# Performance work log

Hardware: AMD Instinct MI355X
Metric: run time of the kernel (lower is better)

## Reference

```python
import jax, jax.numpy as jnp
import numpy as np

N = 10000            # nodes
E = 320000           # edges (avg degree 32)
L = 4                # layers
S = 64               # hidden 0e multiplicity
V = 16               # hidden 1o multiplicity
EMB = 32             # node-attr embedding dim
NB = 8               # bessel basis per channel (r and v -> 2*NB edge feats)
MR = 2.5             # max_radius
DEG = 32.0           # num_neighbors
GS = S + V           # gate input scalars: 64 scalars + 16 gates
NW = S * 2 + V * 2 + V * 2   # 192 per-edge tensor-product weights
MAXT = 100           # max atom types


def _semi_unitary(K):
    # Newton-Schulz orthogonalization: K^T K -> I (semi-unitary uplift matrix)
    K = K / jnp.linalg.norm(K)
    for _ in range(10):
        K = 1.5 * K - 0.5 * K @ (K.T @ K)
    return K


def _smooth_cutoff(t):
    u = 2.0 * (t - 1.0)
    y = (1.0 - jnp.cos(jnp.pi * u)) * 0.5
    return jnp.where(u > 0, 0.0, jnp.where(u < -1.0, 1.0, y))


def _edge_geom(d):
    # d: (E,3) edge vector. Returns cutoff-weighted 1x1o SH (component norm) and bessel features.
    r = jnp.linalg.norm(d, axis=1)                       # (E,)
    sh = np.sqrt(3.0) * d / r[:, None]                   # spherical harmonics 1x1o
    attr = _smooth_cutoff(r / MR)[:, None] * sh          # (E,3)
    k = jnp.arange(1, NB + 1, dtype=jnp.float32) * jnp.pi
    feat = np.sqrt(2.0 / MR) * jnp.sin(k * (r / MR)[:, None]) / r[:, None]
    return attr, feat * np.sqrt(NB)                      # (E,3), (E,NB)


def _fctp(s, v, attr, Ws, Wv):
    # FullyConnectedTensorProduct with pure-scalar (0e) node attr == attr-weighted per-irrep linear
    os = jnp.einsum('ni,ne,oie->no', s, attr, Ws) / np.sqrt(s.shape[1] * EMB)
    ov = jnp.einsum('nim,ne,oie->nom', v, attr, Wv) / np.sqrt(v.shape[1] * EMB)
    return os, ov


def _forward(x, node_attr, edge_src, edge_dst, emb_table, PU_K, h, mix,
             si_Ws, si_Wv, sc_Ws, sc_Wv, lin1_Ws, lin1_Wv, lin2_Ws, lin2_Wv,
             fc_W1, fc_b1, fc_W2, fc_b2, fc_W3, fc_b3):
    attr = emb_table[node_attr]                          # (N,EMB)
    K = _semi_unitary(PU_K)                              # (V,2)
    yv = jnp.einsum('ui,nim->num', K, x.reshape(N, 2, 3))  # uplift vectors
    ys = jnp.zeros((N, S), x.dtype)
    ys_old, yv_old = ys, yv
    c_s, c_x = np.sin(np.pi / 8), np.cos(np.pi / 8)
    for i in range(L):
        ar, fr = _edge_geom(x[:, :3][edge_src] - x[:, :3][edge_dst])
        av, fv = _edge_geom(x[:, 3:][edge_src] - x[:, 3:][edge_dst])
        a = jnp.stack([ar, av], axis=1)                  # (E,2,3) = 2x1o edge attr
        ef = jnp.concatenate([fr, fv], axis=1)           # (E,2*NB)
        # radial MLP -> per-edge TP weights
        hd = jax.nn.silu(ef @ fc_W1[i] + fc_b1[i])
        hd = jax.nn.silu(hd @ fc_W2[i] + fc_b2[i])
        w = hd @ fc_W3[i] + fc_b3[i]                     # (E,NW)
        w1 = w[:, :S * 2].reshape(-1, S, 2)
        w2 = w[:, S * 2:S * 2 + V * 2].reshape(-1, V, 2)
        w3 = w[:, S * 2 + V * 2:].reshape(-1, V, 2)
        # conv: lin1 -> gather -> TP -> scatter -> lin2 ; plus self-connection
        fs, fvv = _fctp(ys, yv, attr, lin1_Ws[i], lin1_Wv[i])
        s_src, v_src = fs[edge_src], fvv[edge_src]
        # 0e x 1o -> 1o (uvu)
        o1 = jnp.einsum('euv,eu,evm->eum', w1, s_src, a) / np.sqrt(2.0)   # (E,S,3)
        # 1o x 1o -> 0e (uvu)
        dots = jnp.einsum('eum,evm->euv', v_src, a)
        o2 = jnp.einsum('euv,euv->eu', w2, dots) / np.sqrt(6.0)           # (E,V)
        # 1o x 1o -> 1o (cross, uvu)
        cr = jnp.cross(v_src[:, :, None, :], a[:, None, :, :])            # (E,V,2,3)
        o3 = jnp.einsum('euv,euvm->eum', w3, cr) / 2.0                    # (E,V,3)
        mid_s = jax.ops.segment_sum(o2, edge_dst, num_segments=N) / np.sqrt(DEG)
        mid_v = jax.ops.segment_sum(jnp.concatenate([o1, o3], axis=1), edge_dst,
                                    num_segments=N) / np.sqrt(DEG)        # (N,S+V,3)
        cs2, cv2 = _fctp(mid_s, mid_v, attr, lin2_Ws[i], lin2_Wv[i])      # (N,GS),(N,V,3)
        scs, scv = _fctp(ys, yv, attr, sc_Ws[i], sc_Wv[i])
        conv_s = c_s * scs + c_x * cs2
        conv_v = c_s * scv + c_x * cv2
        # gate: silu scalars, sigmoid gates * gated vectors
        gns = jax.nn.silu(conv_s[:, :S])
        gnv = jax.nn.sigmoid(conv_s[:, S:])[:, :, None] * conv_v
        # self-interaction: per-irrep linear
        sis = ys @ si_Ws[i].T / np.sqrt(S)
        siv = jnp.einsum('oi,nim->nom', si_Wv[i], yv) / np.sqrt(V)
        # leapfrog update
        h2 = h[i] ** 2
        ns = 2.0 * ys - ys_old + h2 * (mix[i] * gns + (mix[i] - 1.0) * sis)
        nv = 2.0 * yv - yv_old + h2 * (mix[i] * gnv + (mix[i] - 1.0) * siv)
        ys_old, yv_old = ys, yv
        ys, yv = ns, nv
        x = jnp.einsum('ui,num->nim', K, yv).reshape(N, 6)   # project
    return x


def setup_inputs() -> dict:
    key = jax.random.key(0)
    ks = jax.random.split(key, 24)
    def g(i, sh, fan=1.0):
        return jax.random.normal(ks[i], sh, dtype=jnp.float32) / np.sqrt(fan)
    edge_src = jax.random.randint(ks[20], (E,), 0, N, dtype=jnp.int32)
    off = jax.random.randint(ks[21], (E,), 1, N, dtype=jnp.int32)
    edge_dst = (edge_src + off) % N                      # guarantees src != dst
    return {
        'x': g(0, (N, 6)),
        'batch': jnp.zeros((N,), jnp.int32),
        'node_attr': jax.random.randint(ks[22], (N,), 0, MAXT, dtype=jnp.int32),
        'edge_src': edge_src,
        'edge_dst': edge_dst,
        'emb_table': g(1, (MAXT, EMB)),
        'PU_K': g(2, (V, 2)),
        'h': jnp.full((L,), 0.01, jnp.float32),
        'mix': jnp.full((L,), 0.5, jnp.float32),
        'si_Ws': g(3, (L, S, S)), 'si_Wv': g(4, (L, V, V)),
        'sc_Ws': g(5, (L, GS, S, EMB)), 'sc_Wv': g(6, (L, V, V, EMB)),
        'lin1_Ws': g(7, (L, S, S, EMB)), 'lin1_Wv': g(8, (L, V, V, EMB)),
        'lin2_Ws': g(9, (L, GS, V, EMB)), 'lin2_Wv': g(10, (L, V, S + V, EMB)),
        'fc_W1': g(11, (L, 2 * NB, 64), 2 * NB), 'fc_b1': jnp.zeros((L, 64), jnp.float32),
        'fc_W2': g(12, (L, 64, 64), 64), 'fc_b2': jnp.zeros((L, 64), jnp.float32),
        'fc_W3': g(13, (L, 64, NW), 64), 'fc_b3': jnp.zeros((L, NW), jnp.float32),
    }


def reference(x, batch, node_attr, edge_src, edge_dst, emb_table, PU_K, h, mix,
              si_Ws, si_Wv, sc_Ws, sc_Wv, lin1_Ws, lin1_Wv, lin2_Ws, lin2_Wv,
              fc_W1, fc_b1, fc_W2, fc_b2, fc_W3, fc_b3):
    return _forward(x, node_attr, edge_src, edge_dst, emb_table, PU_K, h, mix,
                    si_Ws, si_Wv, sc_Ws, sc_Wv, lin1_Ws, lin1_Wv, lin2_Ws, lin2_Wv,
                    fc_W1, fc_b1, fc_W2, fc_b2, fc_W3, fc_b3)
```

## Files before the change

### kernel.cpp

```cpp
#include <hip/hip_runtime.h>
#include <hip/hip_fp8.h>
#include <math.h>

#define NN 10000
#define NE 320000
#define PI_F 3.14159265358979323846f

typedef __attribute__((ext_vector_type(8))) short short8x;
typedef __attribute__((ext_vector_type(4))) float float4x;
typedef __attribute__((ext_vector_type(4))) unsigned short ushort4x;

#if defined(__has_builtin)
#if __has_builtin(__builtin_amdgcn_cvt_pk_fp8_f32) && __has_builtin(__builtin_amdgcn_cvt_f32_fp8)
#define HW_FP8 1
#endif
#endif

__device__ __forceinline__ unsigned short f2b(float f) {
    unsigned b = __float_as_uint(f);
    return (unsigned short)((b + 0x7FFFu + ((b >> 16) & 1u)) >> 16);
}
__device__ __forceinline__ float b2f(unsigned short u) {
    return __uint_as_float(((unsigned)u) << 16);
}
__device__ __forceinline__ float silu(float x) {
    return x / (1.f + __expf(-x));
}
__device__ __forceinline__ unsigned char f2e4(float f) {
#ifdef HW_FP8
    int r = __builtin_amdgcn_cvt_pk_fp8_f32(f, f, 0, false);
    return (unsigned char)(r & 0xff);
#else
    __hip_fp8_e4m3 q(f);
    return (unsigned char)q.__x;
#endif
}
__device__ __forceinline__ float e42f(unsigned char v) {
#ifdef HW_FP8
    return __builtin_amdgcn_cvt_f32_fp8((int)v, 0);
#else
    __hip_fp8_e4m3 q;
    q.__x = (__hip_fp8_storage_t)v;
    return (float)q;
#endif
}
__device__ __forceinline__ float e4sel(unsigned word, int sel) {
#ifdef HW_FP8
    switch (sel & 3) {
        case 0:  return __builtin_amdgcn_cvt_f32_fp8((int)word, 0);
        case 1:  return __builtin_amdgcn_cvt_f32_fp8((int)word, 1);
        case 2:  return __builtin_amdgcn_cvt_f32_fp8((int)word, 2);
        default: return __builtin_amdgcn_cvt_f32_fp8((int)word, 3);
    }
#else
    return e42f((unsigned char)((word >> (8*(sel & 3))) & 0xffu));
#endif
}
__device__ __forceinline__ unsigned pk4(float a, float b, float c, float d) {
#ifdef HW_FP8
    unsigned w = (unsigned)__builtin_amdgcn_cvt_pk_fp8_f32(a, b, 0, false);
    w = (unsigned)__builtin_amdgcn_cvt_pk_fp8_f32(c, d, (int)w, true);
    return w;
#else
    return (unsigned)f2e4(a) | ((unsigned)f2e4(b) << 8) |
           ((unsigned)f2e4(c) << 16) | ((unsigned)f2e4(d) << 24);
#endif
}

__global__ void k_newton_kernel(const float* __restrict__ PU, float* __restrict__ Kout)
{
    if (threadIdx.x != 0 || blockIdx.x != 0) return;
    float K[32];
    float nrm = 0.f;
    for (int i = 0; i < 32; ++i) { K[i] = PU[i]; nrm += K[i]*K[i]; }
    float inv = 1.0f / sqrtf(nrm);
    for (int i = 0; i < 32; ++i) K[i] *= inv;
    for (int it = 0; it < 10; ++it) {
        float m00 = 0.f, m01 = 0.f, m11 = 0.f;
        for (int u = 0; u < 16; ++u) {
            float a = K[2*u], b = K[2*u+1];
            m00 += a*a; m01 += a*b; m11 += b*b;
        }
        for (int u = 0; u < 16; ++u) {
            float a = K[2*u], b = K[2*u+1];
            K[2*u]   = 1.5f*a - 0.5f*(a*m00 + b*m01);
            K[2*u+1] = 1.5f*b - 0.5f*(a*m01 + b*m11);
        }
    }
    for (int i = 0; i < 32; ++i) Kout[i] = K[i];
}

__global__ __launch_bounds__(256) void init_all_kernel(
    const float* __restrict__ x, const float* __restrict__ K,
    float* __restrict__ xp, float* __restrict__ yv0, float* __restrict__ yv1,
    float* __restrict__ ys0, float* __restrict__ ys1, float* __restrict__ fsb)
{
    int tid = blockIdx.x*256 + threadIdx.x;
    if (tid < NN*8) {
        int n = tid >> 3, c = tid & 7;
        xp[tid] = (c < 6) ? x[n*6 + c] : 0.f;
        return;
    }
    int t2 = tid - NN*8;
    if (t2 < NN*48) {
        int n = t2/48, j = t2%48, u = j/3, m = j%3;
        float v = K[2*u]*x[n*6+m] + K[2*u+1]*x[n*6+3+m];
        yv0[t2] = v; yv1[t2] = v;
        return;
    }
    t2 -= NN*48;
    if (t2 < NN*64) { ys0[t2] = 0.f; ys1[t2] = 0.f; fsb[t2] = 0.f; }
}

__global__ void init_fvv_kernel(const float* __restrict__ yv, const int* __restrict__ types,
                                const float* __restrict__ lin1vT0, float* __restrict__ fvv)
{
    int tid = blockIdx.x*blockDim.x + threadIdx.x;
    if (tid >= NN*48) return;
    int n = tid/48, j = tid%48, o = j/3, m = j%3;
    int t = types[n];
    const float* W = lin1vT0 + (size_t)t*256;
    float acc = 0.f;
    #pragma unroll
    for (int i = 0; i < 16; ++i) acc += yv[n*48 + i*3 + m]*W[i*16 + o];
    fvv[tid] = acc;
}

__device__ __forceinline__ void be_body(const float* __restrict__ W, const float* __restrict__ emb,
                                        float* __restrict__ out, int id, int O, int I, float scale)
{
    int o = id % O; int r = id / O;
    int i = r % I; r /= I;
    int t = r % 100; int l = r / 100;
    const float* w  = W + (((size_t)l*O + o)*I + i)*32;
    const float* em = emb + (size_t)t*32;
    float acc = 0.f;
    #pragma unroll
    for (int e = 0; e < 32; ++e) acc += w[e]*em[e];
    out[id] = acc*scale;
}

#define PREP_TOTAL (2048000 + 1638400 + 512000 + 512000 + 102400 + 102400 + 49152 + 16384 + 16384 + 8192 + 1024)
__global__ __launch_bounds__(256) void prep_kernel(
    const float* __restrict__ lin1_Ws, const float* __restrict__ lin1_Wv,
    const float* __restrict__ sc_Ws,   const float* __restrict__ sc_Wv,
    const float* __restrict__ lin2_Ws, const float* __restrict__ lin2_Wv,
    const float* __restrict__ si_Ws,   const float* __restrict__ si_Wv,
    const float* __restrict__ fc_W1,   const float* __restrict__ fc_W2,
    const float* __restrict__ fc_W3,   const float* __restrict__ emb,
    float* __restrict__ lin1sT, float* __restrict__ lin1vT,
    float* __restrict__ scsT,   float* __restrict__ scvT,
    float* __restrict__ lin2sT, float* __restrict__ lin2vT,
    float* __restrict__ siWsT,  float* __restrict__ siWvT,
    unsigned short* __restrict__ w1bp, unsigned short* __restrict__ w2bp,
    unsigned short* __restrict__ w3bf)
{
    const float s2048 = 0.022097086912079608f;
    const float s512  = 0.044194173824159216f;
    const float s2560 = 0.019764235376052372f;
    int tid = blockIdx.x*256 + threadIdx.x;
    if (tid < 2048000) { be_body(sc_Ws,   emb, scsT,   tid, 80, 64, s2048); return; }
    tid -= 2048000;
    if (tid < 1638400) { be_body(lin1_Ws, emb, lin1sT, tid, 64, 64, s2048); return; }
    tid -= 1638400;
    if (tid < 512000)  { be_body(lin2_Ws, emb, lin2sT, tid, 80, 16, s512);  return; }
    tid -= 512000;
    if (tid < 512000)  { be_body(lin2_Wv, emb, lin2vT, tid, 16, 80, s2560); return; }
    tid -= 512000;
    if (tid < 102400)  { be_body(lin1_Wv, emb, lin1vT, tid, 16, 16, s512);  return; }
    tid -= 102400;
    if (tid < 102400)  { be_body(sc_Wv,   emb, scvT,   tid, 16, 16, s512);  return; }
    tid -= 102400;
    if (tid < 49152) {
        int o = tid % 64; int r = tid / 64; int i = r % 192; int l = r / 192;
        w3bf[tid] = f2b(fc_W3[((size_t)l*64 + o)*192 + i]);
        return;
    }
    tid -= 49152;
    if (tid < 16384) {
        int o = tid % 64; int r = tid / 64; int i = r % 64; int l = r / 64;
        siWsT[tid] = si_Ws[((size_t)l*64 + o)*64 + i]*0.125f;
        return;
    }
    tid -= 16384;
    if (tid < 16384) {
        int kk = tid % 64; int r = tid / 64; int n = r % 64; int l = r / 64;
        w2bp[tid] = f2b(fc_W2[((size_t)l*64 + kk)*64 + n]);
        return;
    }
    tid -= 16384;
    if (tid < 8192) {
        int kk = tid % 32; int r = tid / 32; int n = r % 64; int l = r / 64;
        float v = (kk < 16) ? fc_W1[((size_t)l*16 + kk)*64 + n] : 0.f;
        w1bp[tid] = f2b(v);
        return;
    }
    tid -= 8192;
    if (tid < 1024) {
        int o = tid % 16; int r = tid / 16; int i = r % 16; int l = r / 16;
        siWvT[tid] = si_Wv[((size_t)l*16 + o)*16 + i]*0.25f;
    }
}

__global__ void hist_kernel(const int* __restrict__ dst, int* __restrict__ deg)
{
    int e = blockIdx.x*256 + threadIdx.x;
    if (e < NE) atomicAdd(&deg[dst[e]], 1);
}

__global__ __launch_bounds__(256) void scan_kernel(const int* __restrict__ deg,
                                                   int* __restrict__ segoff,
                                                   int* __restrict__ cursor)
{
    __shared__ int part[256];
    int tid = threadIdx.x;
    int base = tid*40;
    int s = 0;
    for (int i = 0; i < 40; ++i) { int idx = base+i; if (idx < NN) s += deg[idx]; }
    part[tid] = s;
    __syncthreads();
    for (int o = 1; o < 256; o <<= 1) {
        int v = (tid >= o) ? part[tid-o] : 0;
        __syncthreads();
        part[tid] += v;
        __syncthreads();
    }
    int excl = part[tid] - s;
    for (int i = 0; i < 40; ++i) {
        int idx = base+i;
        if (idx < NN) { segoff[idx] = excl; cursor[idx] = excl; excl += deg[idx]; }
        else if (idx == NN) { segoff[NN] = excl; }
    }
}

__global__ void scatter_kernel(const int* __restrict__ src, const int* __restrict__ dst,
                               int* __restrict__ cursor,
                               int* __restrict__ srcs, int* __restrict__ dsts)
{
    int e = blockIdx.x*256 + threadIdx.x;
    if (e >= NE) return;
    int d = dst[e];
    int p = atomicAdd(&cursor[d], 1);
    srcs[p] = src[e]; dsts[p] = d;
}

__global__ __launch_bounds__(256, 5) void edge_fused_kernel(
    const float* __restrict__ xp,
    const int* __restrict__ srcs, const int* __restrict__ dsts,
    const unsigned short* __restrict__ w1b,
    const float* __restrict__ b1,
    const unsigned short* __restrict__ w2b,
    const float* __restrict__ b2,
    const unsigned short* __restrict__ w3b,
    const float* __restrict__ b3,
    const float* __restrict__ fs, const float* __restrict__ fvv,
    float* __restrict__ mid)
{
    __shared__ __align__(16) unsigned char smem[192*68];
    __shared__ unsigned short fsl[64][68];
    __shared__ unsigned short fvl[48][68];
    __shared__ float abuf[6][68];
    __shared__ int sdst[64];
    __shared__ unsigned smaskl[2];
    unsigned short* hbuf = (unsigned short*)smem;
    const float C3f = 0.08838834764831845f;
    int lane = threadIdx.x & 63;
    int wid  = threadIdx.x >> 6;
    int eblk = blockIdx.x * 64;
    int row16 = lane & 15, quad = lane >> 4;
    int erow = 16*wid + row16;

    if (threadIdx.x < 64) {
        int tid = threadIdx.x;
        int own = dsts[eblk + tid];
        int pidx = eblk + tid - ((tid > 0) ? 1 : 0);
        int prev = dsts[pidx];
        sdst[tid] = own;
        bool nb = (tid > 0) && (own != prev);
        unsigned long long bm = __ballot(nb);
        if (tid == 0) { smaskl[0] = (unsigned)bm; smaskl[1] = (unsigned)(bm >> 32); }
    }

    if (lane < 32) {
        int eidx = 16*wid + (lane & 15);
        int half = lane >> 4;
        int p = eblk + eidx;
        int s = srcs[p], d = dsts[p];
        int off = 3*half;
        const float* xs = xp + (size_t)s*8 + off;
        const float* xd = xp + (size_t)d*8 + off;
        float d0 = xs[0]-xd[0], d1 = xs[1]-xd[1], d2 = xs[2]-xd[2];
        float r = sqrtf(d0*d0 + d1*d1 + d2*d2);
        float invr = 1.0f/r;
        float u = 0.8f*r - 2.0f;
        float cut = (u > 0.f) ? 0.f : ((u < -1.f) ? 1.f : 0.5f*(1.f - __cosf(PI_F*u)));
        float sc = 1.7320508075688772f*cut*invr;
        abuf[off+0][eidx] = sc*d0;
        abuf[off+1][eidx] = sc*d1;
        abuf[off+2][eidx] = sc*d2;
        float fsc = 2.5298221281347035f*invr;
        float wr = 1.2566370614359172f*r;
        unsigned epk[4];
        #pragma unroll
        for (int k = 0; k < 4; ++k) {
            float e0 = fsc*__sinf((float)(2*k+1)*wr);
            float e1 = fsc*__sinf((float)(2*k+2)*wr);
            epk[k] = (unsigned)f2b(e0) | ((unsigned)f2b(e1) << 16);
        }
        uint4* hr = (uint4*)(hbuf + eidx*72);
        uint4 q; q.x = epk[0]; q.y = epk[1]; q.z = epk[2]; q.w = epk[3];
        hr[half] = q;
        uint4 qz; qz.x = 0; qz.y = 0; qz.z = 0; qz.w = 0;
        hr[2+half] = qz;
    } else {
        int eidx = 16*wid + (lane & 15);
        int half = (lane >> 4) & 1;
        int s = srcs[eblk + eidx];
        const float4* fp = (const float4*)(fs + (size_t)s*64 + half*32);
        #pragma unroll
        for (int g = 0; g < 8; ++g) {
            float4 t = fp[g];
            int u0 = half*32 + g*4;
            fsl[u0+0][eidx] = f2b(t.x*0.125f);
            fsl[u0+1][eidx] = f2b(t.y*0.125f);
            fsl[u0+2][eidx] = f2b(t.z*0.125f);
            fsl[u0+3][eidx] = f2b(t.w*0.125f);
        }
        const float4* vp = (const float4*)(fvv + (size_t)s*48 + half*24);
        #pragma unroll
        for (int g = 0; g < 6; ++g) {
            float4 t = vp[g];
            int j0 = half*24 + g*4;
            fvl[j0+0][eidx] = f2b(t.x*C3f);
            fvl[j0+1][eidx] = f2b(t.y*C3f);
            fvl[j0+2][eidx] = f2b(t.z*C3f);
            fvl[j0+3][eidx] = f2b(t.w*C3f);
        }
    }

    {
        short8x a = *(const short8x*)(hbuf + erow*72 + quad*8);
        float4x c[4];
        #pragma unroll
        for (int nt = 0; nt < 4; ++nt) {
            short8x b = *(const short8x*)(w1b + ((size_t)(nt*16 + row16))*32 + quad*8);
            c[nt] = __builtin_amdgcn_mfma_f32_16x16x32_bf16(a, b, (float4x){0.f,0.f,0.f,0.f}, 0, 0, 0);
        }
        #pragma unroll
        for (int nt = 0; nt < 4; ++nt) {
            float bias = b1[nt*16 + row16];
            #pragma unroll
            for (int r = 0; r < 4; ++r) {
                float h = silu(c[nt][r] + bias);
                hbuf[(16*wid + quad*4 + r)*72 + nt*16 + row16] = f2b(h);
            }
        }
    }
    {
        short8x a0v = *(const short8x*)(hbuf + erow*72 + 0*32 + quad*8);
        short8x a1v = *(const short8x*)(hbuf + erow*72 + 1*32 + quad*8);
        float4x c[4];
        #pragma unroll
        for (int nt = 0; nt < 4; ++nt) {
            short8x b0 = *(const short8x*)(w2b + ((size_t)(nt*16 + row16))*64 + 0*32 + quad*8);
            float4x t = __builtin_amdgcn_mfma_f32_16x16x32_bf16(a0v, b0, (float4x){0.f,0.f,0.f,0.f}, 0, 0, 0);
            short8x b1v = *(const short8x*)(w2b + ((size_t)(nt*16 + row16))*64 + 1*32 + quad*8);
            c[nt] = __builtin_amdgcn_mfma_f32_16x16x32_bf16(a1v, b1v, t, 0, 0, 0);
        }
        #pragma unroll
        for (int nt = 0; nt < 4; ++nt) {
            float bias = b2[nt*16 + row16];
            #pragma unroll
            for (int r = 0; r < 4; ++r) {
                float h = silu(c[nt][r] + bias);
                hbuf[(16*wid + quad*4 + r)*72 + nt*16 + row16] = f2b(h);
            }
        }
    }
    {
        short8x a0v = *(const short8x*)(hbuf + erow*72 + 0*32 + quad*8);
        short8x a1v = *(const short8x*)(hbuf + erow*72 + 1*32 + quad*8);
        __syncthreads();
        float4x acc[12];
        #pragma unroll
        for (int nt = 0; nt < 12; ++nt) {
            short8x b0 = *(const short8x*)(w3b + ((size_t)(nt*16 + row16))*64 + 0*32 + quad*8);
            float4x t = __builtin_amdgcn_mfma_f32_16x16x32_bf16(a0v, b0, (float4x){0.f,0.f,0.f,0.f}, 0, 0, 0);
            short8x b1v = *(const short8x*)(w3b + ((size_t)(nt*16 + row16))*64 + 1*32 + quad*8);
            acc[nt] = __builtin_amdgcn_mfma_f32_16x16x32_bf16(a1v, b1v, t, 0, 0, 0);
        }
        #pragma unroll
        for (int nt = 0; nt < 12; ++nt) {
            unsigned pw = pk4(acc[nt][0], acc[nt][1], acc[nt][2], acc[nt][3]);
            *(unsigned*)(smem + (size_t)(nt*16 + row16)*68 + 16*wid + quad*4) = pw;
        }
    }
    __syncthreads();

    {
        int c = threadIdx.x;
        unsigned mk0 = __builtin_amdgcn_readfirstlane(smaskl[0]);
        unsigned mk1 = __builtin_amdgcn_readfirstlane(smaskl[1]);
        float acc = 0.f;
        int dcur = sdst[0];
        if (c < 192) {
            int u = c / 3;
            int m = c - 3*u;
            const unsigned char* wra = smem + (size_t)(2*u)*68;
            const unsigned char* wrb = wra + 68;
            const unsigned short* fsr = &fsl[u][0];
            const float* a0r = &abuf[m][0];
            const float* a1r = &abuf[3+m][0];
            float bA = b3[2*u], bB = b3[2*u+1];
            for (int e4 = 0; e4 < 64; e4 += 4) {
                unsigned wa4 = *(const unsigned*)(wra + e4);
                unsigned wb4 = *(const unsigned*)(wrb + e4);
                ushort4x f4v = *(const ushort4x*)(fsr + e4);
                float4x a04 = *(const float4x*)(a0r + e4);
                float4x a14 = *(const float4x*)(a1r + e4);
                float q0 = b2f(f4v[0])*((e4sel(wa4,0)+bA)*a04[0] + (e4sel(wb4,0)+bB)*a14[0]);
                float q1 = b2f(f4v[1])*((e4sel(wa4,1)+bA)*a04[1] + (e4sel(wb4,1)+bB)*a14[1]);
                float q2 = b2f(f4v[2])*((e4sel(wa4,2)+bA)*a04[2] + (e4sel(wb4,2)+bB)*a14[2]);
                float q3 = b2f(f4v[3])*((e4sel(wa4,3)+bA)*a04[3] + (e4sel(wb4,3)+bB)*a14[3]);
                unsigned mch = ((e4 < 32) ? (mk0 >> e4) : (mk1 >> (e4-32))) & 15u;
                if (mch == 0) {
                    acc += (q0 + q1) + (q2 + q3);
                } else {
                    float q[4] = {q0, q1, q2, q3};
                    #pragma unroll
                    for (int k = 0; k < 4; ++k) {
                        if (mch & (1u<<k)) {
                            atomicAdd(&mid[(size_t)dcur*256 + c], acc);
                            acc = 0.f; dcur = sdst[e4+k];
                        }
                        acc += q[k];
                    }
                }
            }
            atomicAdd(&mid[(size_t)dcur*256 + c], acc);
        } else if (c < 208) {
            int u = c - 192;
            const unsigned char* wra = smem + (size_t)(128 + 2*u)*68;
            const unsigned char* wrb = wra + 68;
            const unsigned short* v0r = &fvl[3*u+0][0];
            const unsigned short* v1r = &fvl[3*u+1][0];
            const unsigned short* v2r = &fvl[3*u+2][0];
            float bA = b3[128 + 2*u], bB = b3[129 + 2*u];
            const float FS = 0.8164965809277259f;
            for (int e4 = 0; e4 < 64; e4 += 4) {
                unsigned wa4 = *(const unsigned*)(wra + e4);
                unsigned wb4 = *(const unsigned*)(wrb + e4);
                ushort4x v04 = *(const ushort4x*)(v0r + e4);
                ushort4x v14 = *(const ushort4x*)(v1r + e4);
                ushort4x v24 = *(const ushort4x*)(v2r + e4);
                float4x a00 = *(const float4x*)(&abuf[0][e4]);
                float4x a01 = *(const float4x*)(&abuf[1][e4]);
                float4x a02 = *(const float4x*)(&abuf[2][e4]);
                float4x a10 = *(const float4x*)(&abuf[3][e4]);
                float4x a11 = *(const float4x*)(&abuf[4][e4]);
                float4x a12 = *(const float4x*)(&abuf[5][e4]);
                float q[4];
                #pragma unroll
                for (int k = 0; k < 4; ++k) {
                    float v0 = b2f(v04[k]), v1 = b2f(v14[k]), v2 = b2f(v24[k]);
                    float dd0 = v0*a00[k] + v1*a01[k] + v2*a02[k];
                    float dd1 = v0*a10[k] + v1*a11[k] + v2*a12[k];
                    q[k] = (e4sel(wa4,k)+bA)*dd0 + (e4sel(wb4,k)+bB)*dd1;
                }
                unsigned mch = ((e4 < 32) ? (mk0 >> e4) : (mk1 >> (e4-32))) & 15u;
                if (mch == 0) {
                    acc += (q[0] + q[1]) + (q[2] + q[3]);
                } else {
                    #pragma unroll
                    for (int k = 0; k < 4; ++k) {
                        if (mch & (1u<<k)) {
                            atomicAdd(&mid[(size_t)dcur*256 + c], acc*FS);
                            acc = 0.f; dcur = sdst[e4+k];
                        }
                        acc += q[k];
                    }
                }
            }
            atomicAdd(&mid[(size_t)dcur*256 + c], acc*FS);
        } else {
            int j = c - 208;
            int u = j / 3;
            int m = j - 3*u;
            int m1 = (m == 2) ? 0 : (m + 1);
            int m2 = 3 - m - m1;
            const unsigned char* wra = smem + (size_t)(160 + 2*u)*68;
            const unsigned char* wrb = wra + 68;
            const unsigned short* var = &fvl[3*u+m1][0];
            const unsigned short* vbr = &fvl[3*u+m2][0];
            const float* am1a = &abuf[m1][0];
            const float* am2a = &abuf[m2][0];
            const float* am1b = &abuf[3+m1][0];
            const float* am2b = &abuf[3+m2][0];
            float bA = b3[160 + 2*u], bB = b3[161 + 2*u];
            for (int e4 = 0; e4 < 64; e4 += 4) {
                unsigned wa4 = *(const unsigned*)(wra + e4);
                unsigned wb4 = *(const unsigned*)(wrb + e4);
                ushort4x va4 = *(const ushort4x*)(var + e4);
                ushort4x vb4 = *(const ushort4x*)(vbr + e4);
                float4x a1m1 = *(const float4x*)(am1a + e4);
                float4x a1m2 = *(const float4x*)(am2a + e4);
                float4x a2m1 = *(const float4x*)(am1b + e4);
                float4x a2m2 = *(const float4x*)(am2b + e4);
                float q[4];
                #pragma unroll
                for (int k = 0; k < 4; ++k) {
                    float va = b2f(va4[k]), vb = b2f(vb4[k]);
                    float cx0 = va*a1m2[k] - vb*a1m1[k];
                    float cx1 = va*a2m2[k] - vb*a2m1[k];
                    q[k] = (e4sel(wa4,k)+bA)*cx0 + (e4sel(wb4,k)+bB)*cx1;
                }
                unsigned mch = ((e4 < 32) ? (mk0 >> e4) : (mk1 >> (e4-32))) & 15u;
                if (mch == 0) {
                    acc += (q[0] + q[1]) + (q[2] + q[3]);
                } else {
                    #pragma unroll
                    for (int k = 0; k < 4; ++k) {
                        if (mch & (1u<<k)) {
                            atomicAdd(&mid[(size_t)dcur*256 + c], acc);
                            acc = 0.f; dcur = sdst[e4+k];
                        }
                        acc += q[k];
                    }
                }
            }
            atomicAdd(&mid[(size_t)dcur*256 + c], acc);
        }
    }
}

__global__ __launch_bounds__(256) void node_update_kernel(
    const float* __restrict__ ys, const float* __restrict__ yv,
    float* __restrict__ ys_old, float* __restrict__ yv_old,
    const float* __restrict__ mid,
    const int* __restrict__ types,
    const float* __restrict__ scsT, const float* __restrict__ scvT,
    const float* __restrict__ lin2sT, const float* __restrict__ lin2vT,
    const float* __restrict__ siWsT, const float* __restrict__ siWvT,
    const float* __restrict__ lin1sTn, const float* __restrict__ lin1vTn,
    const float* __restrict__ Kbuf,
    const float* __restrict__ hv, const float* __restrict__ mixv, int layer,
    float* __restrict__ fs_out, float* __restrict__ fvv_out,
    float* __restrict__ xpad, float* __restrict__ dout)
{
    int n = blockIdx.x;
    int lane = threadIdx.x;
    __shared__ float ys_l[64], yv_l[48], mids[16], midv[240];
    __shared__ float conv_s[80], conv_v[48], sis_l[64], siv_l[48], ysn[64], yvn[48];
    int t = types[n];
    {
        float v = mid[(size_t)n*256 + lane];
        if (lane < 192) midv[lane] = v;
        else if (lane < 208) mids[lane-192] = v;
        else midv[192 + (lane-208)] = v;
    }
    if (lane < 64) ys_l[lane] = ys[n*64 + lane];
    else if (lane < 112) yv_l[lane-64] = yv[n*48 + (lane-64)];
    __syncthreads();
    if (lane < 80) {
        const float* Wsc = scsT + (size_t)t*5120;
        const float* W2s = lin2sT + (size_t)t*1280;
        float a_sc = 0.f, a_2 = 0.f;
        #pragma unroll
        for (int i = 0; i < 64; ++i) a_sc += ys_l[i]*Wsc[i*80 + lane];
        #pragma unroll
        for (int i = 0; i < 16; ++i) a_2 += mids[i]*W2s[i*80 + lane];
        conv_s[lane] = 0.3826834323650898f*a_sc + 0.9238795325112867f*a_2;
    } else if (lane < 144) {
        int o = lane - 80;
        float a_si = 0.f;
        #pragma unroll
        for (int i = 0; i < 64; ++i) a_si += ys_l[i]*siWsT[i*64 + o];
        sis_l[o] = a_si;
    } else if (lane < 192) {
        int j = lane - 144, o = j/3, m = j%3;
        const float* Wsc = scvT + (size_t)t*256;
        const float* W2v = lin2vT + (size_t)t*1280;
        float a_sc = 0.f, a_2 = 0.f, a_si = 0.f;
        #pragma unroll
        for (int i = 0; i < 16; ++i) {
            float y = yv_l[i*3+m];
            a_sc += y*Wsc[i*16+o];
            a_si += y*siWvT[i*16+o];
        }
        #pragma unroll
        for (int i = 0; i < 80; ++i) a_2 += midv[i*3+m]*W2v[i*16+o];
        conv_v[j] = 0.3826834323650898f*a_sc + 0.9238795325112867f*a_2;
        siv_l[j] = a_si;
    }
    __syncthreads();
    float hh = hv[layer]; float h2c = hh*hh; float mx = mixv[layer];
    if (lane < 64) {
        float cs = conv_s[lane];
        float gns = cs/(1.f + __expf(-cs));
        float ns = 2.f*ys_l[lane] - ys_old[n*64+lane] + h2c*(mx*gns + (mx-1.f)*sis_l[lane]);
        ys_old[n*64+lane] = ns;
        ysn[lane] = ns;
    } else if (lane < 112) {
        int j = lane-64, o = j/3;
        float g = 1.f/(1.f + __expf(-conv_s[64+o]));
        float gnv = g*conv_v[j];
        float nv = 2.f*yv_l[j] - yv_old[n*48+j] + h2c*(mx*gnv + (mx-1.f)*siv_l[j]);
        yv_old[n*48+j] = nv;
        yvn[j] = nv;
    }
    __syncthreads();
    if (lane < 6) {
        int i = lane/3, m = lane%3;
        float acc = 0.f;
        #pragma unroll
        for (int u = 0; u < 16; ++u) acc += Kbuf[2*u+i]*yvn[u*3+m];
        xpad[n*8 + lane] = acc;
        if (dout) dout[n*6 + lane] = acc;
    }
    if (lane < 64) {
        const float* W = lin1sTn + (size_t)t*4096;
        float acc = 0.f;
        #pragma unroll
        for (int i = 0; i < 64; ++i) acc += ysn[i]*W[i*64 + lane];
        fs_out[n*64 + lane] = acc;
    } else if (lane < 112) {
        int j = lane - 64, o = j/3, m = j%3;
        const float* W = lin1vTn + (size_t)t*256;
        float acc = 0.f;
        #pragma unroll
        for (int i = 0; i < 16; ++i) acc += yvn[i*3+m]*W[i*16 + o];
        fvv_out[n*48 + j] = acc;
    }
}

extern "C" void kernel_launch(void* const* d_in, const int* in_sizes, int n_in,
                              void* d_out, int out_size, void* d_ws, size_t ws_size,
                              hipStream_t stream)
{
    const float* x_in   = (const float*)d_in[0];
    const int*   types  = (const int*)  d_in[2];
    const int*   esrc   = (const int*)  d_in[3];
    const int*   edst   = (const int*)  d_in[4];
    const float* emb    = (const float*)d_in[5];
    const float* PU     = (const float*)d_in[6];
    const float* hv     = (const float*)d_in[7];
    const float* mixv   = (const float*)d_in[8];
    const float* si_Ws  = (const float*)d_in[9];
    const float* si_Wv  = (const float*)d_in[10];
    const float* sc_Ws  = (const float*)d_in[11];
    const float* sc_Wv  = (const float*)d_in[12];
    const float* lin1_Ws= (const float*)d_in[13];
    const float* lin1_Wv= (const float*)d_in[14];
    const float* lin2_Ws= (const float*)d_in[15];
    const float* lin2_Wv= (const float*)d_in[16];
    const float* fc_W1  = (const float*)d_in[17];
    const float* fc_b1  = (const float*)d_in[18];
    const float* fc_W2  = (const float*)d_in[19];
    const float* fc_b2  = (const float*)d_in[20];
    const float* fc_W3  = (const float*)d_in[21];
    const float* fc_b3  = (const float*)d_in[22];

    float* ws = (float*)d_ws;
    size_t off = 0;
    auto alloc = [&](size_t nf) { float* p = ws + off; off += nf; return p; };
    float* Kbuf   = alloc(64);
    float* x_pad  = alloc(80000);
    float* ys0    = alloc(640000);
    float* ys1    = alloc(640000);
    float* yv0    = alloc(480000);
    float* yv1    = alloc(480000);
    float* fsb    = alloc(640000);
    float* fvvb   = alloc(480000);
    float* midb   = alloc((size_t)NN*256);
    float* lin1sT = alloc((size_t)4*100*4096);
    float* lin1vT = alloc((size_t)4*100*256);
    float* scsT   = alloc((size_t)4*100*5120);
    float* scvT   = alloc((size_t)4*100*256);
    float* lin2sT = alloc((size_t)4*100*1280);
    float* lin2vT = alloc((size_t)4*100*1280);
    float* siWsT  = alloc((size_t)4*4096);
    float* siWvT  = alloc((size_t)4*256);
    int* iws = (int*)(ws + off);
    size_t ioff = 0;
    auto ialloc = [&](size_t ni) { int* p = iws + ioff; ioff += ni; return p; };
    int* deg    = ialloc(NN);
    int* segoff = ialloc(NN + 8);
    int* cursor = ialloc(NN);
    int* srcs   = ialloc(NE);
    int* dsts   = ialloc(NE);
    unsigned short* w1bp = (unsigned short*)(iws + ioff);
    unsigned short* w2bp = w1bp + (size_t)4*64*32;
    unsigned short* w3bf = w2bp + (size_t)4*64*64;

    k_newton_kernel<<<1, 1, 0, stream>>>(PU, Kbuf);
    prep_kernel<<<(PREP_TOTAL + 255)/256, 256, 0, stream>>>(
        lin1_Ws, lin1_Wv, sc_Ws, sc_Wv, lin2_Ws, lin2_Wv, si_Ws, si_Wv,
        fc_W1, fc_W2, fc_W3, emb,
        lin1sT, lin1vT, scsT, scvT, lin2sT, lin2vT, siWsT, siWvT,
        w1bp, w2bp, w3bf);
    {
        int tot = NN*8 + NN*48 + NN*64;
        init_all_kernel<<<(tot + 255)/256, 256, 0, stream>>>(
            x_in, Kbuf, x_pad, yv0, yv1, ys0, ys1, fsb);
    }
    init_fvv_kernel<<<(NN*48 + 255)/256, 256, 0, stream>>>(yv0, types, lin1vT, fvvb);

    (void)hipMemsetAsync(deg, 0, NN*sizeof(int), stream);
    hist_kernel<<<(NE+255)/256, 256, 0, stream>>>(edst, deg);
    scan_kernel<<<1, 256, 0, stream>>>(deg, segoff, cursor);
    scatter_kernel<<<(NE+255)/256, 256, 0, stream>>>(esrc, edst, cursor, srcs, dsts);

    float* ys_cur = ys0; float* ys_old = ys1;
    float* yv_cur = yv0; float* yv_old = yv1;
    for (int l = 0; l < 4; ++l) {
        (void)hipMemsetAsync(midb, 0, (size_t)NN*256*sizeof(float), stream);
        edge_fused_kernel<<<NE/64, 256, 0, stream>>>(
            x_pad, srcs, dsts,
            w1bp + (size_t)l*64*32,  fc_b1 + (size_t)l*64,
            w2bp + (size_t)l*64*64,  fc_b2 + (size_t)l*64,
            w3bf + (size_t)l*192*64, fc_b3 + (size_t)l*192,
            fsb, fvvb, midb);
        int ln = (l + 1) & 3;
        node_update_kernel<<<NN, 256, 0, stream>>>(
            ys_cur, yv_cur, ys_old, yv_old,
            midb, types,
            scsT   + (size_t)l*100*5120, scvT   + (size_t)l*100*256,
            lin2sT + (size_t)l*100*1280, lin2vT + (size_t)l*100*1280,
            siWsT  + (size_t)l*4096,     siWvT  + (size_t)l*256,
            lin1sT + (size_t)ln*100*4096, lin1vT + (size_t)ln*100*256,
            Kbuf, hv, mixv, l, fsb, fvvb,
            x_pad, (l == 3) ? (float*)d_out : nullptr);
        float* tmp;
        tmp = ys_cur; ys_cur = ys_old; ys_old = tmp;
        tmp = yv_cur; yv_cur = yv_old; yv_old = tmp;
    }
}
```

Measured before the change: 936.2 us.

## Split edge-message scatter across waves by edge quarter instead of by output channel

The scatter phase used to give each thread one output channel and loop over all 64 edges, so the three channel groups ran divergent code paths. Now each wave handles a 16-edge quarter, and each lane computes all three m components for one scalar channel plus one vector-path channel. This reuses the bf16 feature and weight loads across the three components and shortens the serial loop per thread. In exchange, segments that cross a quarter boundary produce more atomic adds into mid, and the wave still diverges between the iso2 and cross-product branches.

```diff
diff --git a/kernel.cpp b/kernel.cpp
--- a/kernel.cpp
+++ b/kernel.cpp
@@ -398,137 +398,126 @@
     __syncthreads();
 
     {
-        int c = threadIdx.x;
+        int qt = wid;
+        int ebase = 16*qt;
         unsigned mk0 = __builtin_amdgcn_readfirstlane(smaskl[0]);
         unsigned mk1 = __builtin_amdgcn_readfirstlane(smaskl[1]);
-        float acc = 0.f;
-        int dcur = sdst[0];
-        if (c < 192) {
-            int u = c / 3;
-            int m = c - 3*u;
-            const unsigned char* wra = smem + (size_t)(2*u)*68;
-            const unsigned char* wrb = wra + 68;
-            const unsigned short* fsr = &fsl[u][0];
-            const float* a0r = &abuf[m][0];
-            const float* a1r = &abuf[3+m][0];
-            float bA = b3[2*u], bB = b3[2*u+1];
-            for (int e4 = 0; e4 < 64; e4 += 4) {
-                unsigned wa4 = *(const unsigned*)(wra + e4);
-                unsigned wb4 = *(const unsigned*)(wrb + e4);
-                ushort4x f4v = *(const ushort4x*)(fsr + e4);
-                float4x a04 = *(const float4x*)(a0r + e4);
-                float4x a14 = *(const float4x*)(a1r + e4);
-                float q0 = b2f(f4v[0])*((e4sel(wa4,0)+bA)*a04[0] + (e4sel(wb4,0)+bB)*a14[0]);
-                float q1 = b2f(f4v[1])*((e4sel(wa4,1)+bA)*a04[1] + (e4sel(wb4,1)+bB)*a14[1]);
-                float q2 = b2f(f4v[2])*((e4sel(wa4,2)+bA)*a04[2] + (e4sel(wb4,2)+bB)*a14[2]);
-                float q3 = b2f(f4v[3])*((e4sel(wa4,3)+bA)*a04[3] + (e4sel(wb4,3)+bB)*a14[3]);
-                unsigned mch = ((e4 < 32) ? (mk0 >> e4) : (mk1 >> (e4-32))) & 15u;
-                if (mch == 0) {
-                    acc += (q0 + q1) + (q2 + q3);
-                } else {
-                    float q[4] = {q0, q1, q2, q3};
-                    #pragma unroll
-                    for (int k = 0; k < 4; ++k) {
-                        if (mch & (1u<<k)) {
-                            atomicAdd(&mid[(size_t)dcur*256 + c], acc);
-                            acc = 0.f; dcur = sdst[e4+k];
-                        }
-                        acc += q[k];
-                    }
-                }
+        unsigned mkq = (((qt & 2) ? mk1 : mk0) >> (16*(qt & 1))) & 0xffffu;
+        mkq &= ~1u;
+
+        const unsigned char* w1p = smem + (size_t)(2*lane)*68;
+        const unsigned short* f1p = &fsl[lane][0];
+        float b1A = b3[2*lane], b1B = b3[2*lane+1];
+
+        bool iso2 = lane < 16;
+        int j3 = lane - 16;
+        int u3 = j3 / 3;
+        int m3 = j3 - 3*u3;
+        int m1 = (m3 == 2) ? 0 : (m3 + 1);
+        int m2 = 3 - m3 - m1;
+        const unsigned char* wbp;
+        const unsigned short* vAp;
+        const unsigned short* vBp;
+        const unsigned short* vCp;
+        const float* aM1a; const float* aM2a; const float* aM1b; const float* aM2b;
+        float bbA, bbB;
+        if (iso2) {
+            wbp = smem + (size_t)(128 + 2*lane)*68;
+            vAp = &fvl[3*lane+0][0]; vBp = &fvl[3*lane+1][0]; vCp = &fvl[3*lane+2][0];
+            aM1a = aM2a = aM1b = aM2b = &abuf[0][0];
+            bbA = b3[128 + 2*lane]; bbB = b3[129 + 2*lane];
+        } else {
+            wbp = smem + (size_t)(160 + 2*u3)*68;
+            vAp = &fvl[3*u3+m1][0]; vBp = &fvl[3*u3+m2][0]; vCp = &fvl[0][0];
+            aM1a = &abuf[m1][0]; aM2a = &abuf[m2][0];
+            aM1b = &abuf[3+m1][0]; aM2b = &abuf[3+m2][0];
+            bbA = b3[160 + 2*u3]; bbB = b3[161 + 2*u3];
+        }
+        float FSb = iso2 ? 0.8164965809277259f : 1.0f;
+        int cb = 192 + lane;
+
+        float acc0 = 0.f, acc1 = 0.f, acc2 = 0.f, accb = 0.f;
+        int dcur = sdst[ebase];
+
+        #pragma unroll
+        for (int ch = 0; ch < 4; ++ch) {
+            int e4 = ebase + 4*ch;
+            float4x a00 = *(const float4x*)(&abuf[0][e4]);
+            float4x a01 = *(const float4x*)(&abuf[1][e4]);
+            float4x a02 = *(const float4x*)(&abuf[2][e4]);
+            float4x a10 = *(const float4x*)(&abuf[3][e4]);
+            float4x a11 = *(const float4x*)(&abuf[4][e4]);
+            float4x a12 = *(const float4x*)(&abuf[5][e4]);
+            unsigned wa4 = *(const unsigned*)(w1p + e4);
+            unsigned wb4 = *(const unsigned*)(w1p + 68 + e4);
+            ushort4x f4 = *(const ushort4x*)(f1p + e4);
+            float q10[4], q11[4], q12[4];
+            #pragma unroll
+            for (int k = 0; k < 4; ++k) {
+                float f = b2f(f4[k]);
+                float wa = (e4sel(wa4, k) + b1A)*f;
+                float wb = (e4sel(wb4, k) + b1B)*f;
+                q10[k] = wa*a00[k] + wb*a10[k];
+                q11[k] = wa*a01[k] + wb*a11[k];
+                q12[k] = wa*a02[k] + wb*a12[k];
             }
-            atomicAdd(&mid[(size_t)dcur*256 + c], acc);
-        } else if (c < 208) {
-            int u = c - 192;
-            const unsigned char* wra = smem + (size_t)(128 + 2*u)*68;
-            const unsigned char* wrb = wra + 68;
-            const unsigned short* v0r = &fvl[3*u+0][0];
-            const unsigned short* v1r = &fvl[3*u+1][0];
-            const unsigned short* v2r = &fvl[3*u+2][0];
-            float bA = b3[128 + 2*u], bB = b3[129 + 2*u];
-            const float FS = 0.8164965809277259f;
-            for (int e4 = 0; e4 < 64; e4 += 4) {
-                unsigned wa4 = *(const unsigned*)(wra + e4);
-                unsigned wb4 = *(const unsigned*)(wrb + e4);
-                ushort4x v04 = *(const ushort4x*)(v0r + e4);
-                ushort4x v14 = *(const ushort4x*)(v1r + e4);
-                ushort4x v24 = *(const ushort4x*)(v2r + e4);
-                float4x a00 = *(const float4x*)(&abuf[0][e4]);
-                float4x a01 = *(const float4x*)(&abuf[1][e4]);
-                float4x a02 = *(const float4x*)(&abuf[2][e4]);
-                float4x a10 = *(const float4x*)(&abuf[3][e4]);
-                float4x a11 = *(const float4x*)(&abuf[4][e4]);
-                float4x a12 = *(const float4x*)(&abuf[5][e4]);
-                float q[4];
+            float qb[4];
+            unsigned wba4 = *(const unsigned*)(wbp + e4);
+            unsigned wbb4 = *(const unsigned*)(wbp + 68 + e4);
+            if (iso2) {
+                ushort4x v04 = *(const ushort4x*)(vAp + e4);
+                ushort4x v14 = *(const ushort4x*)(vBp + e4);
+                ushort4x v24 = *(const ushort4x*)(vCp + e4);
                 #pragma unroll
                 for (int k = 0; k < 4; ++k) {
                     float v0 = b2f(v04[k]), v1 = b2f(v14[k]), v2 = b2f(v24[k]);
                     float dd0 = v0*a00[k] + v1*a01[k] + v2*a02[k];
                     float dd1 = v0*a10[k] + v1*a11[k] + v2*a12[k];
-                    q[k] = (e4sel(wa4,k)+bA)*dd0 + (e4sel(wb4,k)+bB)*dd1;
+                    qb[k] = (e4sel(wba4,k)+bbA)*dd0 + (e4sel(wbb4,k)+bbB)*dd1;
                 }
-                unsigned mch = ((e4 < 32) ? (mk0 >> e4) : (mk1 >> (e4-32))) & 15u;
-                if (mch == 0) {
-                    acc += (q[0] + q[1]) + (q[2] + q[3]);
-                } else {
-                    #pragma unroll
-                    for (int k = 0; k < 4; ++k) {
-                        if (mch & (1u<<k)) {
-                            atomicAdd(&mid[(size_t)dcur*256 + c], acc*FS);
-                            acc = 0.f; dcur = sdst[e4+k];
-                        }
-                        acc += q[k];
-                    }
-                }
-            }
-            atomicAdd(&mid[(size_t)dcur*256 + c], acc*FS);
-        } else {
-            int j = c - 208;
-            int u = j / 3;
-            int m = j - 3*u;
-            int m1 = (m == 2) ? 0 : (m + 1);
-            int m2 = 3 - m - m1;
-            const unsigned char* wra = smem + (size_t)(160 + 2*u)*68;
-            const unsigned char* wrb = wra + 68;
-            const unsigned short* var = &fvl[3*u+m1][0];
-            const unsigned short* vbr = &fvl[3*u+m2][0];
-            const float* am1a = &abuf[m1][0];
-            const float* am2a = &abuf[m2][0];
-            const float* am1b = &abuf[3+m1][0];
-            const float* am2b = &abuf[3+m2][0];
-            float bA = b3[160 + 2*u], bB = b3[161 + 2*u];
-            for (int e4 = 0; e4 < 64; e4 += 4) {
-                unsigned wa4 = *(const unsigned*)(wra + e4);
-                unsigned wb4 = *(const unsigned*)(wrb + e4);
-                ushort4x va4 = *(const ushort4x*)(var + e4);
-                ushort4x vb4 = *(const ushort4x*)(vbr + e4);
-                float4x a1m1 = *(const float4x*)(am1a + e4);
-                float4x a1m2 = *(const float4x*)(am2a + e4);
-                float4x a2m1 = *(const float4x*)(am1b + e4);
-                float4x a2m2 = *(const float4x*)(am2b + e4);
-                float q[4];
+            } else {
+                ushort4x va4 = *(const ushort4x*)(vAp + e4);
+                ushort4x vb4 = *(const ushort4x*)(vBp + e4);
+                float4x c1m1 = *(const float4x*)(aM1a + e4);
+                float4x c1m2 = *(const float4x*)(aM2a + e4);
+                float4x c2m1 = *(const float4x*)(aM1b + e4);
+                float4x c2m2 = *(const float4x*)(aM2b + e4);
                 #pragma unroll
                 for (int k = 0; k < 4; ++k) {
                     float va = b2f(va4[k]), vb = b2f(vb4[k]);
-                    float cx0 = va*a1m2[k] - vb*a1m1[k];
-                    float cx1 = va*a2m2[k] - vb*a2m1[k];
-                    q[k] = (e4sel(wa4,k)+bA)*cx0 + (e4sel(wb4,k)+bB)*cx1;
-                }
-                unsigned mch = ((e4 < 32) ? (mk0 >> e4) : (mk1 >> (e4-32))) & 15u;
-                if (mch == 0) {
-                    acc += (q[0] + q[1]) + (q[2] + q[3]);
-                } else {
-                    #pragma unroll
-                    for (int k = 0; k < 4; ++k) {
-                        if (mch & (1u<<k)) {
-                            atomicAdd(&mid[(size_t)dcur*256 + c], acc);
-                            acc = 0.f; dcur = sdst[e4+k];
-                        }
-                        acc += q[k];
-                    }
+                    float cx0 = va*c1m2[k] - vb*c1m1[k];
+                    float cx1 = va*c2m2[k] - vb*c2m1[k];
+                    qb[k] = (e4sel(wba4,k)+bbA)*cx0 + (e4sel(wbb4,k)+bbB)*cx1;
                 }
             }
-            atomicAdd(&mid[(size_t)dcur*256 + c], acc);
+            unsigned mch = (mkq >> (4*ch)) & 15u;
+            if (mch == 0) {
+                acc0 += (q10[0] + q10[1]) + (q10[2] + q10[3]);
+                acc1 += (q11[0] + q11[1]) + (q11[2] + q11[3]);
+                acc2 += (q12[0] + q12[1]) + (q12[2] + q12[3]);
+                accb += (qb[0] + qb[1]) + (qb[2] + qb[3]);
+            } else {
+                #pragma unroll
+                for (int k = 0; k < 4; ++k) {
+                    if (mch & (1u << k)) {
+                        float* mrow = mid + (size_t)dcur*256;
+                        atomicAdd(mrow + 3*lane + 0, acc0);
+                        atomicAdd(mrow + 3*lane + 1, acc1);
+                        atomicAdd(mrow + 3*lane + 2, acc2);
+                        atomicAdd(mrow + cb, accb*FSb);
+                        acc0 = acc1 = acc2 = accb = 0.f;
+                        dcur = sdst[e4 + k];
+                    }
+                    acc0 += q10[k]; acc1 += q11[k]; acc2 += q12[k]; accb += qb[k];
+                }
+            }
+        }
+        {
+            float* mrow = mid + (size_t)dcur*256;
+            atomicAdd(mrow + 3*lane + 0, acc0);
+            atomicAdd(mrow + 3*lane + 1, acc1);
+            atomicAdd(mrow + 3*lane + 2, acc2);
+            atomicAdd(mrow + cb, accb*FSb);
         }
     }
 }
```

Result: slower. 1.031 ms (+10.2%).
